# Kernel tuning notes

Hardware: AMD Instinct MI355X
Metric: run time of the kernel (lower is better)

The kernel has to match this reference:

```python
import jax, jax.numpy as jnp
import numpy as np

B, T, D = 8, 1024, 1024
H = 16
HD = D // H
FF = 4 * D
EPS = 1e-5


def _ln(x, gamma, beta):
    # torch.var default is unbiased (ddof=1); MyLayerNorm intended normalization
    mean = jnp.mean(x, axis=-1, keepdims=True)
    var = jnp.var(x, axis=-1, keepdims=True, ddof=1)
    return (x - mean) / jnp.sqrt(var + EPS) * gamma + beta


def setup_inputs() -> dict:
    key = jax.random.key(0)
    ks = jax.random.split(key, 16)
    s = lambda k, shape, fan: jax.random.normal(k, shape, jnp.float32) * (fan ** -0.5)
    return {
        "x": jax.random.normal(ks[0], (B, T, D), jnp.float32),
        "Wq": s(ks[1], (D, D), D), "bq": jnp.zeros((D,), jnp.float32),
        "Wk": s(ks[2], (D, D), D), "bk": jnp.zeros((D,), jnp.float32),
        "Wv": s(ks[3], (D, D), D), "bv": jnp.zeros((D,), jnp.float32),
        "Wo": s(ks[4], (D, D), D), "bo": jnp.zeros((D,), jnp.float32),
        "W1": s(ks[5], (D, FF), D), "b1": jnp.zeros((FF,), jnp.float32),
        "W2": s(ks[6], (FF, D), FF), "b2": jnp.zeros((D,), jnp.float32),
        "g1": jnp.ones((D,), jnp.float32), "be1": jnp.zeros((D,), jnp.float32),
        "g2": jnp.ones((D,), jnp.float32), "be2": jnp.zeros((D,), jnp.float32),
    }


def reference(x, Wq, bq, Wk, bk, Wv, bv, Wo, bo, W1, b1, W2, b2, g1, be1, g2, be2):
    # pre-attention LN
    h = _ln(x, g1, be1)
    # batched QKV (equivalent to concatenated per-head Linears)
    q = (h @ Wq + bq).reshape(B, T, H, HD)
    k = (h @ Wk + bk).reshape(B, T, H, HD)
    v = (h @ Wv + bv).reshape(B, T, H, HD)
    att = jnp.einsum("bthd,bshd->bhts", q, k) * (HD ** -0.5)
    att = jax.nn.softmax(att, axis=-1)
    ctx = jnp.einsum("bhts,bshd->bthd", att, v).reshape(B, T, D)
    h = h + (ctx @ Wo + bo)
    # pre-FFN LN
    h2 = _ln(h, g2, be2)
    ff = jax.nn.gelu(h2 @ W1 + b1, approximate=False) @ W2 + b2
    return h2 + ff
```

## Files before the change

kernel.cpp:

```cpp
#include <hip/hip_runtime.h>
#include <hip/hip_bf16.h>

typedef unsigned short u16;
typedef __attribute__((ext_vector_type(8))) short bf16x8;
typedef __attribute__((ext_vector_type(4))) float floatx4;

__device__ __forceinline__ u16 f2b(float f) {
    union { float f; unsigned int u; } a; a.f = f;
    unsigned int u = a.u;
    unsigned int r = (u + 0x7fffu + ((u >> 16) & 1u)) >> 16;
    return (u16)r;
}
__device__ __forceinline__ float b2f(u16 v) {
    union { unsigned int u; float f; } a; a.u = ((unsigned int)v) << 16;
    return a.f;
}

__device__ __forceinline__ void gload_lds16(const void* g, void* l) {
    auto gp = (const __attribute__((address_space(1))) unsigned int*)g;
    auto lp = (__attribute__((address_space(3))) unsigned int*)l;
    __builtin_amdgcn_global_load_lds(gp, lp, 16, 0, 0);
}

__global__ __launch_bounds__(256) void k_ln_bf(const float* __restrict__ x,
                                               const float* __restrict__ g,
                                               const float* __restrict__ be,
                                               u16* __restrict__ yb) {
    const int row = blockIdx.x;
    const int t = threadIdx.x;
    const float4 xv = ((const float4*)(x + (size_t)row * 1024))[t];
    float s  = xv.x + xv.y + xv.z + xv.w;
    float ss = xv.x * xv.x + xv.y * xv.y + xv.z * xv.z + xv.w * xv.w;
    for (int m = 1; m < 64; m <<= 1) {
        s  += __shfl_xor(s, m);
        ss += __shfl_xor(ss, m);
    }
    __shared__ float sm[8];
    const int wave = t >> 6, lane = t & 63;
    if (lane == 0) { sm[wave] = s; sm[4 + wave] = ss; }
    __syncthreads();
    s  = sm[0] + sm[1] + sm[2] + sm[3];
    ss = sm[4] + sm[5] + sm[6] + sm[7];
    const float mean = s * (1.0f / 1024.0f);
    const float var  = (ss - 1024.0f * mean * mean) * (1.0f / 1023.0f);
    const float rstd = rsqrtf(var + 1e-5f);
    const float4 gv = ((const float4*)g)[t];
    const float4 bv = ((const float4*)be)[t];
    float4 y;
    y.x = (xv.x - mean) * rstd * gv.x + bv.x;
    y.y = (xv.y - mean) * rstd * gv.y + bv.y;
    y.z = (xv.z - mean) * rstd * gv.z + bv.z;
    y.w = (xv.w - mean) * rstd * gv.w + bv.w;
    uint2 pk;
    pk.x = (unsigned int)f2b(y.x) | ((unsigned int)f2b(y.y) << 16);
    pk.y = (unsigned int)f2b(y.z) | ((unsigned int)f2b(y.w) << 16);
    *(uint2*)(yb + (size_t)row * 1024 + t * 4) = pk;
}

__global__ __launch_bounds__(256) void k_tconv(const float* __restrict__ W,
                                               u16* __restrict__ Wt,
                                               int K, int N) {
    __shared__ float tile[32][33];
    const int n0 = blockIdx.x * 32, k0 = blockIdx.y * 32;
    const int tx = threadIdx.x, ty = threadIdx.y;
    for (int i = 0; i < 4; i++) {
        const int kr = ty + i * 8;
        tile[kr][tx] = W[(size_t)(k0 + kr) * N + n0 + tx];
    }
    __syncthreads();
    for (int i = 0; i < 4; i++) {
        const int nr = ty + i * 8;
        Wt[(size_t)(n0 + nr) * K + k0 + tx] = f2b(tile[tx][nr]);
    }
}

__global__ __launch_bounds__(256) void k_tconv4(const float* __restrict__ s0, u16* __restrict__ d0,
                                                const float* __restrict__ s1, u16* __restrict__ d1,
                                                const float* __restrict__ s2, u16* __restrict__ d2,
                                                const float* __restrict__ s3, u16* __restrict__ d3) {
    __shared__ float tile[32][33];
    const float* W; u16* Wt;
    switch (blockIdx.z) {
        case 0: W = s0; Wt = d0; break;
        case 1: W = s1; Wt = d1; break;
        case 2: W = s2; Wt = d2; break;
        default: W = s3; Wt = d3; break;
    }
    const int n0 = blockIdx.x * 32, k0 = blockIdx.y * 32;
    const int tx = threadIdx.x, ty = threadIdx.y;
    for (int i = 0; i < 4; i++) {
        const int kr = ty + i * 8;
        tile[kr][tx] = W[(size_t)(k0 + kr) * 1024 + n0 + tx];
    }
    __syncthreads();
    for (int i = 0; i < 4; i++) {
        const int nr = ty + i * 8;
        Wt[(size_t)(n0 + nr) * 1024 + k0 + tx] = f2b(tile[tx][nr]);
    }
}

__global__ __launch_bounds__(256) void k_vtrans(const u16* __restrict__ v,
                                                u16* __restrict__ vt) {
    __shared__ u16 tile[64][80];
    const int t = threadIdx.x;
    const int t0 = blockIdx.x * 64, hh = blockIdx.y, bb = blockIdx.z;
    const int r = t >> 2, c0 = (t & 3) * 16;
    const u16* src = v + ((size_t)(bb * 1024 + t0 + r)) * 1024 + hh * 64 + c0;
    *(uint4*)&tile[r][c0]     = *(const uint4*)src;
    *(uint4*)&tile[r][c0 + 8] = *(const uint4*)(src + 8);
    __syncthreads();
    const int d = t >> 2;
    u16* dst = vt + (((size_t)(bb * 16 + hh) * 64 + d)) * 1024 + t0 + c0;
    union { u16 s[8]; uint4 v4; } pk;
    for (int j = 0; j < 8; j++) pk.s[j] = tile[c0 + j][d];
    *(uint4*)dst = pk.v4;
    for (int j = 0; j < 8; j++) pk.s[j] = tile[c0 + 8 + j][d];
    *(uint4*)(dst + 8) = pk.v4;
}

template <bool GELU, bool RESID, bool WF32, bool WBF16, bool QKV = false>
__global__ __launch_bounds__(256) void k_gemm(const u16* __restrict__ A,
                                              const u16* __restrict__ Bt,
                                              const float* __restrict__ bias,
                                              const u16* __restrict__ residB,
                                              float* __restrict__ outF,
                                              u16* __restrict__ outB,
                                              int M, int N, int K,
                                              const float* __restrict__ bias2 = nullptr,
                                              const float* __restrict__ bias3 = nullptr) {
    __shared__ __align__(16) u16 S[16896];
    u16* As = S;
    u16* Bs = S + 8192;
    const int t = threadIdx.x;

    const int nb = gridDim.x;
    const int linear = blockIdx.y * nb + blockIdx.x;
    const int per = nb * 8;
    const int gg = linear / per, rr = linear % per;
    const int m0 = (gg * 8 + (rr & 7)) * 128;
    const int n0 = (rr >> 3) * 128;

    const int lane = t & 63, wave = t >> 6;
    const int wm = (wave >> 1) * 64, wn = (wave & 1) * 64;
    const int r16 = lane & 15, quad = lane >> 4;

    floatx4 acc[4][4];
    const floatx4 zero = {0.0f, 0.0f, 0.0f, 0.0f};
    for (int i = 0; i < 4; i++)
        for (int j = 0; j < 4; j++) acc[i][j] = zero;

    const u16* pa[4];
    const u16* pb[4];
    #pragma unroll
    for (int i = 0; i < 4; i++) {
        const int L = t + i * 256;
        const int row = L >> 3, col = L & 7;
        const int gcol = col ^ (row & 7);
        pa[i] = A  + (size_t)(m0 + row) * K + gcol * 8;
        pb[i] = Bt + (size_t)(n0 + row) * K + gcol * 8;
    }

    for (int kk = 0; kk < K; kk += 64) {
        #pragma unroll
        for (int i = 0; i < 4; i++) {
            gload_lds16(pa[i] + kk, As + (t + i * 256) * 8);
            gload_lds16(pb[i] + kk, Bs + (t + i * 256) * 8);
        }
        __syncthreads();

        #pragma unroll
        for (int ks = 0; ks < 2; ks++) {
            bf16x8 af[4], bfr[4];
            #pragma unroll
            for (int i = 0; i < 4; i++) {
                const int ra = wm + i * 16 + r16;
                af[i] = *(const bf16x8*)(As + ra * 64 + (((ks << 2) + quad) ^ (ra & 7)) * 8);
                const int rb = wn + i * 16 + r16;
                bfr[i] = *(const bf16x8*)(Bs + rb * 64 + (((ks << 2) + quad) ^ (rb & 7)) * 8);
            }
            #pragma unroll
            for (int mi = 0; mi < 4; mi++)
                #pragma unroll
                for (int ni = 0; ni < 4; ni++)
                    acc[mi][ni] = __builtin_amdgcn_mfma_f32_16x16x32_bf16(af[mi], bfr[ni], acc[mi][ni], 0, 0, 0);
        }
        __syncthreads();
    }

    const int sect = QKV ? (n0 >> 10) : 0;
    const float* bp = QKV ? (sect == 0 ? bias : (sect == 1 ? bias2 : bias3)) : bias;
    u16* outQ = QKV ? (outB + (size_t)sect * (8192ull * 1024ull)) : outB;

    if (WBF16) {
        u16 (*ct)[132] = (u16(*)[132])S;
        for (int mi = 0; mi < 4; mi++)
            for (int ni = 0; ni < 4; ni++) {
                const int col = wn + ni * 16 + r16;
                const int coln = QKV ? ((n0 + col) & 1023) : (n0 + col);
                const float bv = bp[coln];
                for (int r = 0; r < 4; r++) {
                    const int row = wm + mi * 16 + quad * 4 + r;
                    float v = acc[mi][ni][r] + bv;
                    if (GELU) v = 0.5f * v * (1.0f + erff(v * 0.70710678118654752f));
                    ct[row][col] = f2b(v);
                }
            }
        __syncthreads();
        const int orow = t >> 1, oc = (t & 1) * 64;
        const int grow = m0 + orow;
        u16* dst = QKV ? (outQ + (size_t)grow * 1024 + ((n0 + oc) & 1023))
                       : (outB + (size_t)grow * N + n0 + oc);
        #pragma unroll
        for (int j = 0; j < 8; j++)
            *(uint4*)(dst + j * 8) = *(const uint4*)&ct[orow][oc + j * 8];
    } else {
        for (int mi = 0; mi < 4; mi++)
            for (int ni = 0; ni < 4; ni++) {
                const int gcol = n0 + wn + ni * 16 + r16;
                const float bv = bias[gcol];
                for (int r = 0; r < 4; r++) {
                    const int grow = m0 + wm + mi * 16 + quad * 4 + r;
                    float v = acc[mi][ni][r] + bv;
                    if (GELU) v = 0.5f * v * (1.0f + erff(v * 0.70710678118654752f));
                    const size_t o = (size_t)grow * N + gcol;
                    if (RESID) v += b2f(residB[o]);
                    if (WF32) outF[o] = v;
                }
            }
    }
}

__global__ __launch_bounds__(256) void k_attn_mfma(const u16* __restrict__ q,
                                                   const u16* __restrict__ k,
                                                   const u16* __restrict__ vt,
                                                   u16* __restrict__ ctx) {
    __shared__ u16 Qs[2][64][32];
    __shared__ u16 Ks[2][64][32];
    __shared__ u16 Vs[2][64][32];
    __shared__ u16 Ps[2][64][32];
    const int t = threadIdx.x;
    const int lane = t & 63, wave = t >> 6;
    const int r16 = lane & 15, quad = lane >> 4;
    const int wq = wave * 16;
    const int bx = blockIdx.x;
    const int qt = bx & 15, hh = (bx >> 4) & 15, bb = bx >> 8;
    const size_t qk_base = ((size_t)bb * 1024) * 1024 + hh * 64;
    const size_t vt_base = ((size_t)(bb * 16 + hh) * 64) * 1024;
    const int q0 = qt * 64;

    const int srow = t >> 2, ch = t & 3;
    const int pnl = ch >> 1, soff = (ch & 1) * 16;
    {
        const u16* gp = q + qk_base + (size_t)(q0 + srow) * 1024 + ch * 16;
        *(uint4*)&Qs[pnl][srow][soff]     = *(const uint4*)gp;
        *(uint4*)&Qs[pnl][srow][soff + 8] = *(const uint4*)(gp + 8);
    }

    float m_i[4], l_i[4];
    floatx4 acc_o[4];
    const floatx4 zero = {0.0f, 0.0f, 0.0f, 0.0f};
    for (int r = 0; r < 4; r++) { m_i[r] = -INFINITY; l_i[r] = 0.0f; }
    for (int ni = 0; ni < 4; ni++) acc_o[ni] = zero;

    for (int st = 0; st < 16; st++) {
        __syncthreads();
        const int s0 = st * 64;
        {
            const u16* gk = k + qk_base + (size_t)(s0 + srow) * 1024 + ch * 16;
            *(uint4*)&Ks[pnl][srow][soff]     = *(const uint4*)gk;
            *(uint4*)&Ks[pnl][srow][soff + 8] = *(const uint4*)(gk + 8);
            const u16* gv = vt + vt_base + (size_t)srow * 1024 + s0 + ch * 16;
            *(uint4*)&Vs[pnl][srow][soff]     = *(const uint4*)gv;
            *(uint4*)&Vs[pnl][srow][soff + 8] = *(const uint4*)(gv + 8);
        }
        __syncthreads();

        floatx4 accs[4];
        for (int ni = 0; ni < 4; ni++) accs[ni] = zero;
        for (int ks = 0; ks < 2; ks++) {
            const bf16x8 af = *(const bf16x8*)&Qs[ks][wq + r16][quad * 8];
            for (int ni = 0; ni < 4; ni++) {
                const bf16x8 bf = *(const bf16x8*)&Ks[ks][ni * 16 + r16][quad * 8];
                accs[ni] = __builtin_amdgcn_mfma_f32_16x16x32_bf16(af, bf, accs[ni], 0, 0, 0);
            }
        }

        for (int r = 0; r < 4; r++) {
            float sv[4];
            float mx = -INFINITY;
            for (int ni = 0; ni < 4; ni++) {
                sv[ni] = accs[ni][r] * 0.125f;
                mx = fmaxf(mx, sv[ni]);
            }
            for (int m = 1; m < 16; m <<= 1) mx = fmaxf(mx, __shfl_xor(mx, m));
            const float mn = fmaxf(m_i[r], mx);
            const float al = __expf(m_i[r] - mn);
            float ps = 0.0f;
            u16 pb[4];
            for (int ni = 0; ni < 4; ni++) {
                const float p = __expf(sv[ni] - mn);
                ps += p;
                pb[ni] = f2b(p);
            }
            for (int m = 1; m < 16; m <<= 1) ps += __shfl_xor(ps, m);
            l_i[r] = l_i[r] * al + ps;
            m_i[r] = mn;
            for (int ni = 0; ni < 4; ni++) acc_o[ni][r] *= al;
            const int prow = wq + quad * 4 + r;
            for (int ni = 0; ni < 4; ni++)
                Ps[ni >> 1][prow][(ni & 1) * 16 + r16] = pb[ni];
        }

        for (int ks = 0; ks < 2; ks++) {
            const bf16x8 af = *(const bf16x8*)&Ps[ks][wq + r16][quad * 8];
            for (int ni = 0; ni < 4; ni++) {
                const bf16x8 bf = *(const bf16x8*)&Vs[ks][ni * 16 + r16][quad * 8];
                acc_o[ni] = __builtin_amdgcn_mfma_f32_16x16x32_bf16(af, bf, acc_o[ni], 0, 0, 0);
            }
        }
    }

    for (int r = 0; r < 4; r++) {
        const float inv = 1.0f / l_i[r];
        const size_t rowoff = qk_base + (size_t)(q0 + wq + quad * 4 + r) * 1024;
        for (int ni = 0; ni < 4; ni++)
            ctx[rowoff + ni * 16 + r16] = f2b(acc_o[ni][r] * inv);
    }
}

extern "C" void kernel_launch(void* const* d_in, const int* in_sizes, int n_in,
                              void* d_out, int out_size, void* d_ws, size_t ws_size,
                              hipStream_t stream) {
    const float* x   = (const float*)d_in[0];
    const float* Wq  = (const float*)d_in[1];
    const float* bq  = (const float*)d_in[2];
    const float* Wk  = (const float*)d_in[3];
    const float* bk  = (const float*)d_in[4];
    const float* Wv  = (const float*)d_in[5];
    const float* bv  = (const float*)d_in[6];
    const float* Wo  = (const float*)d_in[7];
    const float* bo  = (const float*)d_in[8];
    const float* W1  = (const float*)d_in[9];
    const float* b1  = (const float*)d_in[10];
    const float* W2  = (const float*)d_in[11];
    const float* b2  = (const float*)d_in[12];
    const float* g1  = (const float*)d_in[13];
    const float* be1 = (const float*)d_in[14];
    const float* g2  = (const float*)d_in[15];
    const float* be2 = (const float*)d_in[16];
    float* out = (float*)d_out;

    const size_t MB = 1ull << 20;
    char* ws = (char*)d_ws;
    u16*   h_b    = (u16*)(ws + 0);
    u16*   qkv_b  = (u16*)(ws + 16 * MB);
    u16*   q_b    = qkv_b;
    u16*   k_b    = (u16*)(ws + 32 * MB);
    u16*   v_b    = (u16*)(ws + 48 * MB);
    u16*   vt_b   = (u16*)(ws + 64 * MB);
    u16*   ctx_b  = (u16*)(ws + 80 * MB);
    float* hres   = (float*)(ws + 96 * MB);
    u16*   h2_b   = (u16*)(ws + 128 * MB);
    u16*   g_b    = (u16*)(ws + 16 * MB);
    u16*   wqkv_t = (u16*)(ws + 160 * MB);
    u16*   wo_t   = (u16*)(ws + 166 * MB);
    u16*   w1_t   = (u16*)(ws + 168 * MB);
    u16*   w2_t   = (u16*)(ws + 176 * MB);
    const int M = 8192, D = 1024, FF = 4096;
    const dim3 tb(32, 8);

    k_tconv4<<<dim3(32, 32, 4), tb, 0, stream>>>(Wq, wqkv_t,
                                                 Wk, wqkv_t + 1024 * 1024,
                                                 Wv, wqkv_t + 2 * 1024 * 1024,
                                                 Wo, wo_t);
    k_tconv<<<dim3(128, 32), tb, 0, stream>>>(W1, w1_t, D, FF);
    k_tconv<<<dim3(32, 128), tb, 0, stream>>>(W2, w2_t, FF, D);

    k_ln_bf<<<M, 256, 0, stream>>>(x, g1, be1, h_b);

    k_gemm<false, false, false, true, true><<<dim3(24, 64), 256, 0, stream>>>(
        h_b, wqkv_t, bq, nullptr, nullptr, qkv_b, M, 3072, D, bk, bv);

    k_vtrans<<<dim3(16, 16, 8), 256, 0, stream>>>(v_b, vt_b);

    k_attn_mfma<<<2048, 256, 0, stream>>>(q_b, k_b, vt_b, ctx_b);

    k_gemm<false, true, true, false><<<dim3(8, 64), 256, 0, stream>>>(
        ctx_b, wo_t, bo, h_b, hres, nullptr, M, D, D);

    k_ln_bf<<<M, 256, 0, stream>>>(hres, g2, be2, h2_b);

    k_gemm<true, false, false, true><<<dim3(32, 64), 256, 0, stream>>>(
        h2_b, w1_t, b1, nullptr, nullptr, g_b, M, FF, D);

    k_gemm<false, true, true, false><<<dim3(8, 64), 256, 0, stream>>>(
        g_b, w2_t, b2, h2_b, out, nullptr, M, D, FF);
}
```

Measured before the change: 605.6 us.

## Prefetch next K/V tile into registers and keep Q fragments in registers

The attention kernel now loads each wave's Q fragments straight into registers instead of staging them through shared memory. The next K/V tile is prefetched into registers while MFMA and softmax run on the current tile. Shared-memory rows are padded from 32 to 40 elements to reduce bank conflicts, and the inner loops are explicitly unrolled. The aim is to hide global load latency and cut LDS traffic, at the cost of extra registers and a redundant wrap-around prefetch on the last iteration.

```diff
diff --git a/kernel.cpp b/kernel.cpp
--- a/kernel.cpp
+++ b/kernel.cpp
@@ -234,10 +234,9 @@
                                                    const u16* __restrict__ k,
                                                    const u16* __restrict__ vt,
                                                    u16* __restrict__ ctx) {
-    __shared__ u16 Qs[2][64][32];
-    __shared__ u16 Ks[2][64][32];
-    __shared__ u16 Vs[2][64][32];
-    __shared__ u16 Ps[2][64][32];
+    __shared__ u16 Ks[2][64][40];
+    __shared__ u16 Vs[2][64][40];
+    __shared__ u16 Ps[2][64][40];
     const int t = threadIdx.x;
     const int lane = t & 63, wave = t >> 6;
     const int r16 = lane & 15, quad = lane >> 4;
@@ -248,13 +247,22 @@
     const size_t vt_base = ((size_t)(bb * 16 + hh) * 64) * 1024;
     const int q0 = qt * 64;
 
+    bf16x8 qf[2];
+    {
+        const u16* qp = q + qk_base + (size_t)(q0 + wq + r16) * 1024 + quad * 8;
+        qf[0] = *(const bf16x8*)qp;
+        qf[1] = *(const bf16x8*)(qp + 32);
+    }
+
     const int srow = t >> 2, ch = t & 3;
     const int pnl = ch >> 1, soff = (ch & 1) * 16;
-    {
-        const u16* gp = q + qk_base + (size_t)(q0 + srow) * 1024 + ch * 16;
-        *(uint4*)&Qs[pnl][srow][soff]     = *(const uint4*)gp;
-        *(uint4*)&Qs[pnl][srow][soff + 8] = *(const uint4*)(gp + 8);
-    }
+    const u16* gkb = k + qk_base + (size_t)srow * 1024 + ch * 16;
+    const u16* gvb = vt + vt_base + (size_t)srow * 1024 + ch * 16;
+
+    uint4 k0v = *(const uint4*)gkb;
+    uint4 k1v = *(const uint4*)(gkb + 8);
+    uint4 v0v = *(const uint4*)gvb;
+    uint4 v1v = *(const uint4*)(gvb + 8);
 
     float m_i[4], l_i[4];
     floatx4 acc_o[4];
@@ -263,28 +271,32 @@
     for (int ni = 0; ni < 4; ni++) acc_o[ni] = zero;
 
     for (int st = 0; st < 16; st++) {
+        *(uint4*)&Ks[pnl][srow][soff]     = k0v;
+        *(uint4*)&Ks[pnl][srow][soff + 8] = k1v;
+        *(uint4*)&Vs[pnl][srow][soff]     = v0v;
+        *(uint4*)&Vs[pnl][srow][soff + 8] = v1v;
         __syncthreads();
-        const int s0 = st * 64;
-        {
-            const u16* gk = k + qk_base + (size_t)(s0 + srow) * 1024 + ch * 16;
-            *(uint4*)&Ks[pnl][srow][soff]     = *(const uint4*)gk;
-            *(uint4*)&Ks[pnl][srow][soff + 8] = *(const uint4*)(gk + 8);
-            const u16* gv = vt + vt_base + (size_t)srow * 1024 + s0 + ch * 16;
-            *(uint4*)&Vs[pnl][srow][soff]     = *(const uint4*)gv;
-            *(uint4*)&Vs[pnl][srow][soff + 8] = *(const uint4*)(gv + 8);
-        }
-        __syncthreads();
+
+        const int sn = (st + 1) & 15;
+        const u16* gk = gkb + (size_t)sn * 65536;
+        const u16* gv = gvb + sn * 64;
+        const uint4 kn0 = *(const uint4*)gk;
+        const uint4 kn1 = *(const uint4*)(gk + 8);
+        const uint4 vn0 = *(const uint4*)gv;
+        const uint4 vn1 = *(const uint4*)(gv + 8);
 
         floatx4 accs[4];
         for (int ni = 0; ni < 4; ni++) accs[ni] = zero;
+        #pragma unroll
         for (int ks = 0; ks < 2; ks++) {
-            const bf16x8 af = *(const bf16x8*)&Qs[ks][wq + r16][quad * 8];
-            for (int ni = 0; ni < 4; ni++) {
-                const bf16x8 bf = *(const bf16x8*)&Ks[ks][ni * 16 + r16][quad * 8];
-                accs[ni] = __builtin_amdgcn_mfma_f32_16x16x32_bf16(af, bf, accs[ni], 0, 0, 0);
+            #pragma unroll
+            for (int ni = 0; ni < 4; ni++) {
+                const bf16x8 bfr = *(const bf16x8*)&Ks[ks][ni * 16 + r16][quad * 8];
+                accs[ni] = __builtin_amdgcn_mfma_f32_16x16x32_bf16(qf[ks], bfr, accs[ni], 0, 0, 0);
             }
         }
 
+        #pragma unroll
         for (int r = 0; r < 4; r++) {
             float sv[4];
             float mx = -INFINITY;
@@ -311,13 +323,18 @@
                 Ps[ni >> 1][prow][(ni & 1) * 16 + r16] = pb[ni];
         }
 
+        #pragma unroll
         for (int ks = 0; ks < 2; ks++) {
             const bf16x8 af = *(const bf16x8*)&Ps[ks][wq + r16][quad * 8];
+            #pragma unroll
             for (int ni = 0; ni < 4; ni++) {
                 const bf16x8 bf = *(const bf16x8*)&Vs[ks][ni * 16 + r16][quad * 8];
                 acc_o[ni] = __builtin_amdgcn_mfma_f32_16x16x32_bf16(af, bf, acc_o[ni], 0, 0, 0);
             }
         }
+
+        k0v = kn0; k1v = kn1; v0v = vn0; v1v = vn1;
+        __syncthreads();
     }
 
     for (int r = 0; r < 4; r++) {
```

Measured after the change: 578.9 us. -4.4%, faster.
